# Kernel tuning notes

Hardware: AMD Instinct MI355X
Metric: run time of the kernel (lower is better)

Reference implementation:

```python
import jax, jax.numpy as jnp
import numpy as np

N, IN_FEATS, HIDDEN, N_CLASSES = 12000, 256, 256, 40
EPS = 1e-12  # F.normalize default eps


def setup_inputs() -> dict:
    key = jax.random.key(0)
    ks = jax.random.split(key, 6)
    # dense adjacency, scaled like a row-normalized graph operator
    adj = jax.random.uniform(ks[0], (N, N), jnp.float32) * (1.0 / 64.0)
    x = jax.random.normal(ks[1], (N, IN_FEATS), jnp.float32)
    # xavier-uniform-like weights, zero biases (matches init_params)
    def xavier(k, fan_in, fan_out):
        lim = np.sqrt(6.0 / (fan_in + fan_out)).astype(np.float32)
        return jax.random.uniform(k, (fan_in, fan_out), jnp.float32, -lim, lim)
    W0 = xavier(ks[2], IN_FEATS, HIDDEN)
    W1 = xavier(ks[3], HIDDEN, HIDDEN)
    W2 = xavier(ks[4], HIDDEN, N_CLASSES)
    b0 = jnp.zeros((HIDDEN,), jnp.float32)
    b1 = jnp.zeros((HIDDEN,), jnp.float32)
    b2 = jnp.zeros((N_CLASSES,), jnp.float32)
    return {"adj": adj, "x": x, "W0": W0, "b0": b0, "W1": W1, "b1": b1, "W2": W2, "b2": b2}


def _l2_normalize(h):
    # F.normalize(h): rows divided by max(||row||_2, eps)
    norm = jnp.sqrt(jnp.sum(h * h, axis=1, keepdims=True))
    return h / jnp.maximum(norm, EPS)


def reference(adj, x, W0, b0, W1, b1, W2, b2):
    # layer 0: aggregate -> linear -> bias -> relu -> l2-normalize (dropout=eval identity)
    h = _l2_normalize(jax.nn.relu((adj @ x) @ W0 + b0))
    # layer 1 (hidden)
    h = _l2_normalize(jax.nn.relu((adj @ h) @ W1 + b1))
    # output layer: no activation / normalize / dropout
    h = (adj @ h) @ W2 + b2
    return h
```

## Files before the change

### kernel.cpp

```cpp
#include <hip/hip_runtime.h>
#include <hip/hip_bf16.h>

#define M_ROWS 12000
#define K_PAD  12032
#define FEAT   256
#define NCLS   40
#define NSLICE 5
#define NTILES 188
#define NBM    47
#define PSLABE (M_ROWS * FEAT)
#define TILE_SHORTS 16384
#define HALF_SHORTS 8192

typedef __attribute__((ext_vector_type(4))) float f32x4;
typedef __attribute__((ext_vector_type(8))) short s16x8;
typedef __attribute__((ext_vector_type(4))) short s16x4;
typedef unsigned int u32;

__device__ __forceinline__ short f2bf(float f){
  __hip_bfloat16 h = __float2bfloat16(f);
  union { __hip_bfloat16 h; short s; } u; u.h = h; return u.s;
}
__device__ __forceinline__ float bf2f(short s){
  union { float f; u32 u; } v; v.u = ((u32)(unsigned short)s) << 16; return v.f;
}

__device__ __forceinline__ f32x4 mfma16(s16x8 a, s16x8 b, f32x4 c){
  return __builtin_amdgcn_mfma_f32_16x16x32_bf16(a, b, c, 0, 0, 0);
}

__device__ __forceinline__ void gl16(const void* g, void* l){
  __builtin_amdgcn_global_load_lds(
      (const __attribute__((address_space(1))) u32*)g,
      (__attribute__((address_space(3))) u32*)l, 16, 0, 0);
}

#define VM6   do { asm volatile("s_waitcnt vmcnt(6)" ::: "memory"); \
                   __builtin_amdgcn_sched_barrier(0); } while(0)
#define VM4   do { asm volatile("s_waitcnt vmcnt(4)" ::: "memory"); \
                   __builtin_amdgcn_sched_barrier(0); } while(0)
#define VM0   do { asm volatile("s_waitcnt vmcnt(0)" ::: "memory"); \
                   __builtin_amdgcn_sched_barrier(0); } while(0)
#define LGK0  do { asm volatile("s_waitcnt lgkmcnt(0)" ::: "memory"); \
                   __builtin_amdgcn_sched_barrier(0); } while(0)
#define BARR  do { __builtin_amdgcn_s_barrier(); \
                   __builtin_amdgcn_sched_barrier(0); } while(0)
#define SBAR  __builtin_amdgcn_sched_barrier(0)

__device__ __forceinline__ int swz(int r){ return (r & 3) ^ ((r >> 2) & 3); }

__global__ __launch_bounds__(256) void k_transpose_pack(const float* __restrict__ src,
                                                        short* __restrict__ Bpack){
  const int t = threadIdx.x;
  if (blockIdx.x == 375){
    short* d = Bpack + (size_t)187 * TILE_SHORTS + HALF_SHORTS + t * 32;
    s16x8 z = (s16x8)0;
    #pragma unroll
    for (int i = 0; i < 4; ++i) *(s16x8*)(d + 8*i) = z;
    return;
  }
  __shared__ float tile[32][257];
  const int r0 = blockIdx.x * 32;
  {
    const int r = t >> 3, cs = (t & 7) * 32;
    const float* s = src + (size_t)(r0 + r) * FEAT + cs;
    #pragma unroll
    for (int i = 0; i < 8; ++i){
      f32x4 v = *(const f32x4*)(s + 4*i);
      tile[r][cs + 4*i + 0] = v[0];
      tile[r][cs + 4*i + 1] = v[1];
      tile[r][cs + 4*i + 2] = v[2];
      tile[r][cs + 4*i + 3] = v[3];
    }
  }
  __syncthreads();
  const int c = t;
  const int kt = r0 >> 6, hh = (r0 >> 5) & 1, sc = swz(c);
  short* d = Bpack + (size_t)kt * TILE_SHORTS + hh * HALF_SHORTS + c * 32;
  #pragma unroll
  for (int i = 0; i < 4; ++i){
    s16x8 o;
    #pragma unroll
    for (int j = 0; j < 8; ++j) o[j] = f2bf(tile[8*i + j][c]);
    *(s16x8*)(d + ((i ^ sc) * 8)) = o;
  }
}

__global__ __launch_bounds__(512, 2) void k_gemm_l0(const float* __restrict__ adj,
                                                    const short* __restrict__ Bpack,
                                                    short* __restrict__ Apack,
                                                    short* __restrict__ Pbase){
  __shared__ __align__(16) short lds[2][4][8192];

  const int t = threadIdx.x;
  const int w = t >> 6, l = t & 63;
  const int wm = w >> 2, wn = w & 3;
  const int lr = l & 15, lg = l >> 4;

  int id = blockIdx.x;
  {
    const int xcd = id & 7, idx = id >> 3;
    id = (xcd < 3 ? xcd * 30 : 90 + (xcd - 3) * 29) + idx;
  }
  const int bm = id % NBM, s = id / NBM;
  const int row0 = bm * 256;
  const int u0  = (s < 3) ? s * 38 : 114 + (s - 3) * 37;
  const int nst = (s < 3) ? 38 : 37;

  const char* Bb = (const char*)Bpack;
  const size_t tp = (size_t)t * 16;
  short* Aw = Apack + (size_t)bm * NTILES * TILE_SHORTS;

  size_t abase[2];
  #pragma unroll
  for (int p = 0; p < 2; ++p){
    const int si = p * 512 + t;
    const int r  = si >> 2, sl = si & 3;
    int grow = row0 + r; if (grow > M_ROWS - 1) grow = M_ROWS - 1;
    abase[p] = (size_t)grow * M_ROWS + (size_t)((sl ^ swz(r)) * 8);
  }

  f32x4 av0[4], av1[4];

#define ISSUE_A0(kt) do{ \
    av0[0] = *(const f32x4*)(adj + abase[0] + (kt)*64);      \
    av0[1] = *(const f32x4*)(adj + abase[0] + (kt)*64 + 4);  \
    av0[2] = *(const f32x4*)(adj + abase[1] + (kt)*64);      \
    av0[3] = *(const f32x4*)(adj + abase[1] + (kt)*64 + 4); }while(0)
#define ISSUE_A1(kt) do{ \
    av1[0] = *(const f32x4*)(adj + abase[0] + (kt)*64 + 32);     \
    av1[1] = *(const f32x4*)(adj + abase[0] + (kt)*64 + 32 + 4); \
    av1[2] = *(const f32x4*)(adj + abase[1] + (kt)*64 + 32);     \
    av1[3] = *(const f32x4*)(adj + abase[1] + (kt)*64 + 32 + 4); }while(0)

#define CVT_WRITE_A(q, h, kt, AV) do{                                         \
    _Pragma("unroll")                                                         \
    for (int p = 0; p < 2; ++p){                                              \
      s16x8 o;                                                                \
      _Pragma("unroll")                                                       \
      for (int j = 0; j < 4; ++j){ o[j] = f2bf(AV[2*p][j]); o[4+j] = f2bf(AV[2*p+1][j]); } \
      const int si = p * 512 + t;                                             \
      *(s16x8*)&lds[q][h][si * 8] = o;                                        \
      *(s16x8*)(Aw + (size_t)(kt) * TILE_SHORTS + (h) * HALF_SHORTS + si * 8) = o; \
    } }while(0)

#define ST_BH(q, h, kt) do{                                                   \
    const char* s_ = Bb + (size_t)(kt) * 32768 + (h) * 16384 + tp;            \
    gl16(s_,        (char*)&lds[q][2+(h)][0] + w*1024);                       \
    gl16(s_ + 8192, (char*)&lds[q][2+(h)][0] + 8192 + w*1024); }while(0)

#define AF(q, h, mf) \
    (*(const s16x8*)&lds[q][h][ (wm*128 + (mf)*16 + lr) * 32 + \
      ((lg ^ swz(wm*128 + (mf)*16 + lr)) * 8) ])
#define BF(q, h, nf) \
    (*(const s16x8*)&lds[q][2+(h)][ (wn*64 + (nf)*16 + lr) * 32 + \
      ((lg ^ swz(wn*64 + (nf)*16 + lr)) * 8) ])

  f32x4 acc[8][4];
  #pragma unroll
  for (int m = 0; m < 8; ++m)
    #pragma unroll
    for (int n = 0; n < 4; ++n) acc[m][n] = (f32x4)(0.0f);

  ISSUE_A0(u0); ST_BH(0, 0, u0);
  ISSUE_A1(u0); ST_BH(0, 1, u0);
  VM6;  CVT_WRITE_A(0, 0, u0, av0);
  VM0;  CVT_WRITE_A(0, 1, u0, av1);
  LGK0;
  BARR;

  for (int t2 = 0; t2 < nst; ++t2){
    const int q = t2 & 1, qn = q ^ 1;
    const bool stg = (t2 + 1 < nst);
    const int ktn = u0 + t2 + 1;

    s16x8 bfr[4], af[4];

    #pragma unroll
    for (int n = 0; n < 4; ++n) bfr[n] = BF(q, 0, n);
    #pragma unroll
    for (int m = 0; m < 4; ++m) af[m] = AF(q, 0, m);
    if (stg){ ISSUE_A0(ktn); ST_BH(qn, 0, ktn); }
    BARR;
    __builtin_amdgcn_s_setprio(1);
    #pragma unroll
    for (int m = 0; m < 4; ++m)
      #pragma unroll
      for (int n = 0; n < 4; ++n)
        acc[m][n] = mfma16(af[m], bfr[n], acc[m][n]);
    __builtin_amdgcn_s_setprio(0);
    BARR;

    #pragma unroll
    for (int m = 0; m < 4; ++m) af[m] = AF(q, 0, m + 4);
    if (stg){ ISSUE_A1(ktn); ST_BH(qn, 1, ktn); }
    BARR;
    __builtin_amdgcn_s_setprio(1);
    #pragma unroll
    for (int m = 0; m < 4; ++m)
      #pragma unroll
      for (int n = 0; n < 4; ++n)
        acc[m + 4][n] = mfma16(af[m], bfr[n], acc[m + 4][n]);
    __builtin_amdgcn_s_setprio(0);
    BARR;

    #pragma unroll
    for (int n = 0; n < 4; ++n) bfr[n] = BF(q, 1, n);
    #pragma unroll
    for (int m = 0; m < 4; ++m) af[m] = AF(q, 1, m);
    if (stg){ VM6; CVT_WRITE_A(qn, 0, ktn, av0); }
    BARR;
    __builtin_amdgcn_s_setprio(1);
    #pragma unroll
    for (int m = 0; m < 4; ++m)
      #pragma unroll
      for (int n = 0; n < 4; ++n)
        acc[m][n] = mfma16(af[m], bfr[n], acc[m][n]);
    __builtin_amdgcn_s_setprio(0);
    BARR;

    #pragma unroll
    for (int m = 0; m < 4; ++m) af[m] = AF(q, 1, m + 4);
    if (stg){ VM0; CVT_WRITE_A(qn, 1, ktn, av1); }
    BARR;
    __builtin_amdgcn_s_setprio(1);
    #pragma unroll
    for (int m = 0; m < 4; ++m)
      #pragma unroll
      for (int n = 0; n < 4; ++n)
        acc[m + 4][n] = mfma16(af[m], bfr[n], acc[m + 4][n]);
    __builtin_amdgcn_s_setprio(0);
    if (stg) LGK0;
    BARR;
  }
#undef ISSUE_A0
#undef ISSUE_A1
#undef CVT_WRITE_A
#undef ST_BH
#undef AF
#undef BF

  short* P = Pbase + (size_t)s * PSLABE;
  #pragma unroll
  for (int m = 0; m < 8; ++m){
    const int row = row0 + wm*128 + m*16 + lg*4;
    #pragma unroll
    for (int n = 0; n < 4; ++n){
      const int col = wn*64 + n*16 + lr;
      short* pp = P + (size_t)row * FEAT + col;
      #pragma unroll
      for (int r = 0; r < 4; ++r)
        if (row + r < M_ROWS) pp[(size_t)r * FEAT] = f2bf(acc[m][n][r]);
    }
  }
}

__global__ __launch_bounds__(512, 2) void k_gemm_la2(const short* __restrict__ Apack,
                                                     const short* __restrict__ Bpack,
                                                     short* __restrict__ Pbase){
  __shared__ __align__(16) short Alds[3][16384];
  __shared__ __align__(16) short Blds[3][8192];

  const int t = threadIdx.x;
  const int w = t >> 6, l = t & 63;
  const int wm = w >> 2, wn = w & 3;
  const int lr = l & 15, lg = l >> 4;

  int id = blockIdx.x;
  {
    const int xcd = id & 7, idx = id >> 3;
    id = (xcd < 3 ? xcd * 30 : 90 + (xcd - 3) * 29) + idx;
  }
  const int bm = id % NBM, s = id / NBM;
  const int row0 = bm * 256;
  const int u0  = (s < 3) ? s * 38 : 114 + (s - 3) * 37;
  const int nst = (s < 3) ? 38 : 37;

  const char* Ab = (const char*)(Apack + (size_t)bm * NTILES * TILE_SHORTS);
  const char* Bb = (const char*)Bpack;
  const size_t tp = (size_t)t * 16;

#define ST_AH(buf, kt, h) do{                                                 \
    const char* s_ = Ab + (size_t)(kt) * 32768 + (h) * 16384 + tp;            \
    gl16(s_,        (char*)&Alds[buf][(h)*8192] + w*1024);                    \
    gl16(s_ + 8192, (char*)&Alds[buf][(h)*8192] + 8192 + w*1024); }while(0)
#define ST_BH(buf, kt, h) do{                                                 \
    const char* s_ = Bb + (size_t)(kt) * 32768 + (h) * 16384 + tp;            \
    gl16(s_,        (char*)&Blds[buf][0] + w*1024);                           \
    gl16(s_ + 8192, (char*)&Blds[buf][0] + 8192 + w*1024); }while(0)

#define AF(buf, h, mf) \
    (*(const s16x8*)&Alds[buf][ (h)*8192 + (wm*128 + (mf)*16 + lr) * 32 + \
      ((lg ^ swz(wm*128 + (mf)*16 + lr)) * 8) ])
#define BF(buf, nf) \
    (*(const s16x8*)&Blds[buf][ (wn*64 + (nf)*16 + lr) * 32 + \
      ((lg ^ swz(wn*64 + (nf)*16 + lr)) * 8) ])

  f32x4 acc[8][4];
  #pragma unroll
  for (int m = 0; m < 8; ++m)
    #pragma unroll
    for (int n = 0; n < 4; ++n) acc[m][n] = (f32x4)(0.0f);

  ST_AH(0, u0, 0); ST_AH(0, u0, 1);
  SBAR;
  ST_BH(0, u0, 0); ST_BH(1, u0, 1);
  SBAR;
  if (nst > 1){ ST_AH(1, u0 + 1, 0); ST_AH(1, u0 + 1, 1); VM4; }
  else        { VM0; }
  BARR;

  for (int t2 = 0; t2 < nst; ++t2){
    const int a0 = t2 % 3;
    const int b0 = (2*t2) % 3, b1 = (2*t2 + 1) % 3;
    const bool s1 = (t2 + 1 < nst), s2 = (t2 + 2 < nst);
    const int kt1 = u0 + t2 + 1, kt2 = u0 + t2 + 2;

    s16x8 bfr[4], af[8];

    #pragma unroll
    for (int n = 0; n < 4; ++n) bfr[n] = BF(b0, n);
    #pragma unroll
    for (int m = 0; m < 8; ++m) af[m] = AF(a0, 0, m);
    if (s1) ST_BH((2*t2 + 2) % 3, kt1, 0);
    BARR;
    __builtin_amdgcn_s_setprio(1);
    #pragma unroll
    for (int m = 0; m < 8; ++m)
      #pragma unroll
      for (int n = 0; n < 4; ++n)
        acc[m][n] = mfma16(af[m], bfr[n], acc[m][n]);
    __builtin_amdgcn_s_setprio(0);
    BARR;

    #pragma unroll
    for (int n = 0; n < 4; ++n) bfr[n] = BF(b1, n);
    #pragma unroll
    for (int m = 0; m < 8; ++m) af[m] = AF(a0, 1, m);
    if (s1) ST_BH((2*t2 + 3) % 3, kt1, 1);
    SBAR;
    if (s2){ ST_AH((t2 + 2) % 3, kt2, 0); ST_AH((t2 + 2) % 3, kt2, 1); }
    BARR;
    __builtin_amdgcn_s_setprio(1);
    #pragma unroll
    for (int m = 0; m < 8; ++m)
      #pragma unroll
      for (int n = 0; n < 4; ++n)
        acc[m][n] = mfma16(af[m], bfr[n], acc[m][n]);
    __builtin_amdgcn_s_setprio(0);
    if (s2)      { VM4; }
    else if (s1) { VM0; }
    BARR;
  }
#undef ST_AH
#undef ST_BH
#undef AF
#undef BF

  short* P = Pbase + (size_t)s * PSLABE;
  #pragma unroll
  for (int m = 0; m < 8; ++m){
    const int row = row0 + wm*128 + m*16 + lg*4;
    #pragma unroll
    for (int n = 0; n < 4; ++n){
      const int col = wn*64 + n*16 + lr;
      short* pp = P + (size_t)row * FEAT + col;
      #pragma unroll
      for (int r = 0; r < 4; ++r)
        if (row + r < M_ROWS) pp[(size_t)r * FEAT] = f2bf(acc[m][n][r]);
    }
  }
}

__global__ __launch_bounds__(256) void k_fused2(const short* __restrict__ Pb,
                                                const float* __restrict__ W,
                                                const float* __restrict__ b,
                                                short* __restrict__ Bpack){
  __shared__ float ylds[32][257];
  __shared__ float red[32][33];
  __shared__ float scale[32];
  const int t  = threadIdx.x;
  const int r0 = blockIdx.x * 32;
  {
    const int r = t >> 3, cs = (t & 7) * 32;
    const size_t off = (size_t)(r0 + r) * FEAT + cs;
    float aa[32];
    {
      const short* p0 = Pb + off;
      #pragma unroll
      for (int i4 = 0; i4 < 4; ++i4){
        s16x8 v = *(const s16x8*)(p0 + i4*8);
        #pragma unroll
        for (int e = 0; e < 8; ++e) aa[i4*8 + e] = bf2f(v[e]);
      }
    }
    #pragma unroll
    for (int s = 1; s < NSLICE; ++s){
      const short* ps = Pb + (size_t)s * PSLABE + off;
      #pragma unroll
      for (int i4 = 0; i4 < 4; ++i4){
        s16x8 v = *(const s16x8*)(ps + i4*8);
        #pragma unroll
        for (int e = 0; e < 8; ++e) aa[i4*8 + e] += bf2f(v[e]);
      }
    }
    #pragma unroll
    for (int k = 0; k < 32; ++k) ylds[r][cs + k] = aa[k];
  }
  __syncthreads();

  const int rg = t >> 5;
  const int cg = t & 31;
  float acc[4][8];
  {
    float bias[8];
    #pragma unroll
    for (int j = 0; j < 8; ++j) bias[j] = b[cg*8 + j];
    #pragma unroll
    for (int i = 0; i < 4; ++i)
      #pragma unroll
      for (int j = 0; j < 8; ++j) acc[i][j] = bias[j];
  }

  #pragma unroll 4
  for (int k = 0; k < FEAT; ++k){
    float yv[4];
    #pragma unroll
    for (int i = 0; i < 4; ++i) yv[i] = ylds[rg*4 + i][k];
    f32x4 w0 = *(const f32x4*)(W + (size_t)k * FEAT + cg*8);
    f32x4 w1 = *(const f32x4*)(W + (size_t)k * FEAT + cg*8 + 4);
    #pragma unroll
    for (int i = 0; i < 4; ++i){
      #pragma unroll
      for (int j = 0; j < 4; ++j){
        acc[i][j]     += yv[i] * w0[j];
        acc[i][4 + j] += yv[i] * w1[j];
      }
    }
  }

  #pragma unroll
  for (int i = 0; i < 4; ++i){
    float ss = 0.0f;
    #pragma unroll
    for (int j = 0; j < 8; ++j){
      float v = fmaxf(acc[i][j], 0.0f);
      acc[i][j] = v;
      ss += v * v;
    }
    red[rg*4 + i][cg] = ss;
  }
  __syncthreads();
  if (t < 32){
    float ssum = 0.0f;
    #pragma unroll
    for (int j = 0; j < 32; ++j) ssum += red[t][j];
    scale[t] = 1.0f / fmaxf(sqrtf(ssum), 1e-12f);
  }
  __syncthreads();

  float sc[4];
  #pragma unroll
  for (int i = 0; i < 4; ++i) sc[i] = scale[rg*4 + i];

  const int kb   = r0 + rg * 4;
  const int kt   = kb >> 6, hh = (kb >> 5) & 1, g = (kb >> 3) & 3, e0 = kb & 7;
  short* dbase = Bpack + (size_t)kt * TILE_SHORTS + hh * HALF_SHORTS;
  #pragma unroll
  for (int j = 0; j < 8; ++j){
    const int c = cg * 8 + j;
    s16x4 o;
    #pragma unroll
    for (int i = 0; i < 4; ++i) o[i] = f2bf(acc[i][j] * sc[i]);
    *(s16x4*)(dbase + c * 32 + ((g ^ swz(c)) * 8) + e0) = o;
  }
}

__global__ __launch_bounds__(256) void k_final2(const short* __restrict__ Pb,
                                                const float* __restrict__ W2,
                                                const float* __restrict__ b2,
                                                float* __restrict__ out){
  __shared__ float ylds[32][257];
  const int t  = threadIdx.x;
  const int r0 = blockIdx.x * 32;
  {
    const int r = t >> 3, cs = (t & 7) * 32;
    const size_t off = (size_t)(r0 + r) * FEAT + cs;
    float aa[32];
    {
      const short* p0 = Pb + off;
      #pragma unroll
      for (int i4 = 0; i4 < 4; ++i4){
        s16x8 v = *(const s16x8*)(p0 + i4*8);
        #pragma unroll
        for (int e = 0; e < 8; ++e) aa[i4*8 + e] = bf2f(v[e]);
      }
    }
    #pragma unroll
    for (int s = 1; s < NSLICE; ++s){
      const short* ps = Pb + (size_t)s * PSLABE + off;
      #pragma unroll
      for (int i4 = 0; i4 < 4; ++i4){
        s16x8 v = *(const s16x8*)(ps + i4*8);
        #pragma unroll
        for (int e = 0; e < 8; ++e) aa[i4*8 + e] += bf2f(v[e]);
      }
    }
    #pragma unroll
    for (int k = 0; k < 32; ++k) ylds[r][cs + k] = aa[k];
  }
  __syncthreads();

  #pragma unroll
  for (int e = t; e < 32 * NCLS; e += 256){
    const int r = e / NCLS, n = e % NCLS;
    float a = b2[n];
    #pragma unroll 8
    for (int k = 0; k < FEAT; ++k)
      a = fmaf(ylds[r][k], W2[(size_t)k * NCLS + n], a);
    out[(size_t)(r0 + r) * NCLS + n] = a;
  }
}

extern "C" void kernel_launch(void* const* d_in, const int* in_sizes, int n_in,
                              void* d_out, int out_size, void* d_ws, size_t ws_size,
                              hipStream_t stream){
  const float* adj = (const float*)d_in[0];
  const float* x   = (const float*)d_in[1];
  const float* W0  = (const float*)d_in[2];
  const float* b0  = (const float*)d_in[3];
  const float* W1  = (const float*)d_in[4];
  const float* b1  = (const float*)d_in[5];
  const float* W2  = (const float*)d_in[6];
  const float* b2  = (const float*)d_in[7];
  float* out = (float*)d_out;

  char* ws = (char*)d_ws;
  const size_t BPACK_BYTES = (size_t)NTILES * TILE_SHORTS * 2;
  const size_t APACK_BYTES = (size_t)NBM * NTILES * TILE_SHORTS * 2;

  short* Bpack = (short*)ws;
  short* Apack = (short*)(ws + BPACK_BYTES);
  short* P     = (short*)(ws + BPACK_BYTES + APACK_BYTES);

  const dim3 b256(256), b512(512);

  k_transpose_pack<<<376, b256, 0, stream>>>(x, Bpack);

  k_gemm_l0<<<NBM * NSLICE, b512, 0, stream>>>(adj, Bpack, Apack, P);
  k_fused2<<<375, b256, 0, stream>>>(P, W0, b0, Bpack);
  k_gemm_la2<<<NBM * NSLICE, b512, 0, stream>>>(Apack, Bpack, P);
  k_fused2<<<375, b256, 0, stream>>>(P, W1, b1, Bpack);
  k_gemm_la2<<<NBM * NSLICE, b512, 0, stream>>>(Apack, Bpack, P);
  k_final2<<<375, b256, 0, stream>>>(P, W2, b2, out);
}
```

Baseline: 526.8 us.

## Replace 256-row aggregation GEMM with 64-row tiles and relax layer-0 waits

Measured after the change: 659.7 us. +25.2%, slower.

```diff
diff --git a/kernel.cpp b/kernel.cpp
--- a/kernel.cpp
+++ b/kernel.cpp
@@ -39,13 +39,14 @@
                    __builtin_amdgcn_sched_barrier(0); } while(0)
 #define VM4   do { asm volatile("s_waitcnt vmcnt(4)" ::: "memory"); \
                    __builtin_amdgcn_sched_barrier(0); } while(0)
+#define VM1   do { asm volatile("s_waitcnt vmcnt(1)" ::: "memory"); \
+                   __builtin_amdgcn_sched_barrier(0); } while(0)
 #define VM0   do { asm volatile("s_waitcnt vmcnt(0)" ::: "memory"); \
                    __builtin_amdgcn_sched_barrier(0); } while(0)
 #define LGK0  do { asm volatile("s_waitcnt lgkmcnt(0)" ::: "memory"); \
                    __builtin_amdgcn_sched_barrier(0); } while(0)
 #define BARR  do { __builtin_amdgcn_s_barrier(); \
                    __builtin_amdgcn_sched_barrier(0); } while(0)
-#define SBAR  __builtin_amdgcn_sched_barrier(0)
 
 __device__ __forceinline__ int swz(int r){ return (r & 3) ^ ((r >> 2) & 3); }
 
@@ -165,7 +166,7 @@
   ISSUE_A0(u0); ST_BH(0, 0, u0);
   ISSUE_A1(u0); ST_BH(0, 1, u0);
   VM6;  CVT_WRITE_A(0, 0, u0, av0);
-  VM0;  CVT_WRITE_A(0, 1, u0, av1);
+  VM4;  CVT_WRITE_A(0, 1, u0, av1);
   LGK0;
   BARR;
 
@@ -204,11 +205,12 @@
     __builtin_amdgcn_s_setprio(0);
     BARR;
 
+    if (stg) { VM6; } else { VM4; }
     #pragma unroll
     for (int n = 0; n < 4; ++n) bfr[n] = BF(q, 1, n);
     #pragma unroll
     for (int m = 0; m < 4; ++m) af[m] = AF(q, 1, m);
-    if (stg){ VM6; CVT_WRITE_A(qn, 0, ktn, av0); }
+    if (stg){ CVT_WRITE_A(qn, 0, ktn, av0); }
     BARR;
     __builtin_amdgcn_s_setprio(1);
     #pragma unroll
@@ -221,7 +223,7 @@
 
     #pragma unroll
     for (int m = 0; m < 4; ++m) af[m] = AF(q, 1, m + 4);
-    if (stg){ VM0; CVT_WRITE_A(qn, 1, ktn, av1); }
+    if (stg){ VM4; CVT_WRITE_A(qn, 1, ktn, av1); }
     BARR;
     __builtin_amdgcn_s_setprio(1);
     #pragma unroll
@@ -255,115 +257,100 @@
   }
 }
 
-__global__ __launch_bounds__(512, 2) void k_gemm_la2(const short* __restrict__ Apack,
-                                                     const short* __restrict__ Bpack,
-                                                     short* __restrict__ Pbase){
-  __shared__ __align__(16) short Alds[3][16384];
-  __shared__ __align__(16) short Blds[3][8192];
+__global__ __launch_bounds__(256, 3) void k_gemm32(const short* __restrict__ Apack,
+                                                   const short* __restrict__ Bpack,
+                                                   short* __restrict__ Pbase){
+  __shared__ __align__(16) short Al[3][2048];
+  __shared__ __align__(16) short Bl[2][8192];
 
   const int t = threadIdx.x;
   const int w = t >> 6, l = t & 63;
-  const int wm = w >> 2, wn = w & 3;
   const int lr = l & 15, lg = l >> 4;
 
   int id = blockIdx.x;
   {
     const int xcd = id & 7, idx = id >> 3;
-    id = (xcd < 3 ? xcd * 30 : 90 + (xcd - 3) * 29) + idx;
-  }
-  const int bm = id % NBM, s = id / NBM;
-  const int row0 = bm * 256;
+    id = (xcd < 4 ? xcd * 118 : 472 + (xcd - 4) * 117) + idx;
+  }
+  const int mb = id % 188, s = id / 188;
+  const int bm = mb >> 2, qr = mb & 3;
+  const int row0 = mb * 64;
   const int u0  = (s < 3) ? s * 38 : 114 + (s - 3) * 37;
-  const int nst = (s < 3) ? 38 : 37;
-
-  const char* Ab = (const char*)(Apack + (size_t)bm * NTILES * TILE_SHORTS);
+  const int nstep = ((s < 3) ? 38 : 37) * 2;
+
+  const char* Aq = (const char*)(Apack + (size_t)bm * NTILES * TILE_SHORTS)
+                 + (size_t)qr * 4096;
   const char* Bb = (const char*)Bpack;
-  const size_t tp = (size_t)t * 16;
-
-#define ST_AH(buf, kt, h) do{                                                 \
-    const char* s_ = Ab + (size_t)(kt) * 32768 + (h) * 16384 + tp;            \
-    gl16(s_,        (char*)&Alds[buf][(h)*8192] + w*1024);                    \
-    gl16(s_ + 8192, (char*)&Alds[buf][(h)*8192] + 8192 + w*1024); }while(0)
-#define ST_BH(buf, kt, h) do{                                                 \
-    const char* s_ = Bb + (size_t)(kt) * 32768 + (h) * 16384 + tp;            \
-    gl16(s_,        (char*)&Blds[buf][0] + w*1024);                           \
-    gl16(s_ + 8192, (char*)&Blds[buf][0] + 8192 + w*1024); }while(0)
-
-#define AF(buf, h, mf) \
-    (*(const s16x8*)&Alds[buf][ (h)*8192 + (wm*128 + (mf)*16 + lr) * 32 + \
-      ((lg ^ swz(wm*128 + (mf)*16 + lr)) * 8) ])
-#define BF(buf, nf) \
-    (*(const s16x8*)&Blds[buf][ (wn*64 + (nf)*16 + lr) * 32 + \
-      ((lg ^ swz(wn*64 + (nf)*16 + lr)) * 8) ])
-
-  f32x4 acc[8][4];
-  #pragma unroll
-  for (int m = 0; m < 8; ++m)
+
+#define ST_A(buf, st_) do{                                                    \
+    const int kt_ = u0 + ((st_) >> 1), h_ = (st_) & 1;                        \
+    gl16(Aq + (size_t)kt_ * 32768 + h_ * 16384 + t * 16,                      \
+         (char*)&Al[buf][0] + w * 1024); }while(0)
+#define ST_B(buf, st_) do{                                                    \
+    const char* s_ = Bb + (size_t)(u0 + ((st_) >> 1)) * 32768                 \
+                   + ((st_) & 1) * 16384;                                     \
+    _Pragma("unroll")                                                         \
+    for (int j = 0; j < 4; ++j)                                               \
+      gl16(s_ + (j * 256 + t) * 16, (char*)&Bl[buf][0] + j * 4096 + w * 1024);\
+    }while(0)
+
+#define AF32(buf, mf) \
+    (*(const s16x8*)&Al[buf][ ((mf)*16 + lr) * 32 + \
+      ((lg ^ swz((mf)*16 + lr)) * 8) ])
+#define BF32(buf, nf) \
+    (*(const s16x8*)&Bl[buf][ (w*64 + (nf)*16 + lr) * 32 + \
+      ((lg ^ swz(w*64 + (nf)*16 + lr)) * 8) ])
+
+  f32x4 acc[4][4];
+  #pragma unroll
+  for (int m = 0; m < 4; ++m)
     #pragma unroll
     for (int n = 0; n < 4; ++n) acc[m][n] = (f32x4)(0.0f);
 
-  ST_AH(0, u0, 0); ST_AH(0, u0, 1);
-  SBAR;
-  ST_BH(0, u0, 0); ST_BH(1, u0, 1);
-  SBAR;
-  if (nst > 1){ ST_AH(1, u0 + 1, 0); ST_AH(1, u0 + 1, 1); VM4; }
-  else        { VM0; }
+  ST_A(0, 0);
+  ST_B(0, 0);
+  ST_A(1, 1);
+  VM1;
   BARR;
 
-  for (int t2 = 0; t2 < nst; ++t2){
-    const int a0 = t2 % 3;
-    const int b0 = (2*t2) % 3, b1 = (2*t2 + 1) % 3;
-    const bool s1 = (t2 + 1 < nst), s2 = (t2 + 2 < nst);
-    const int kt1 = u0 + t2 + 1, kt2 = u0 + t2 + 2;
-
-    s16x8 bfr[4], af[8];
-
-    #pragma unroll
-    for (int n = 0; n < 4; ++n) bfr[n] = BF(b0, n);
-    #pragma unroll
-    for (int m = 0; m < 8; ++m) af[m] = AF(a0, 0, m);
-    if (s1) ST_BH((2*t2 + 2) % 3, kt1, 0);
-    BARR;
+  for (int st = 0; st < nstep; ++st){
+    const int q  = st & 1;
+    const int ab = st % 3;
+    const bool s1 = (st + 1 < nstep), s2 = (st + 2 < nstep);
+
+    if (s1) ST_B(q ^ 1, st + 1);
+    if (s2) ST_A((st + 2) % 3, st + 2);
+
+    s16x8 bfr[4], af[4];
+    #pragma unroll
+    for (int n = 0; n < 4; ++n) bfr[n] = BF32(q, n);
+    #pragma unroll
+    for (int m = 0; m < 4; ++m) af[m] = AF32(ab, m);
+
     __builtin_amdgcn_s_setprio(1);
     #pragma unroll
-    for (int m = 0; m < 8; ++m)
+    for (int m = 0; m < 4; ++m)
       #pragma unroll
       for (int n = 0; n < 4; ++n)
         acc[m][n] = mfma16(af[m], bfr[n], acc[m][n]);
     __builtin_amdgcn_s_setprio(0);
-    BARR;
-
-    #pragma unroll
-    for (int n = 0; n < 4; ++n) bfr[n] = BF(b1, n);
-    #pragma unroll
-    for (int m = 0; m < 8; ++m) af[m] = AF(a0, 1, m);
-    if (s1) ST_BH((2*t2 + 3) % 3, kt1, 1);
-    SBAR;
-    if (s2){ ST_AH((t2 + 2) % 3, kt2, 0); ST_AH((t2 + 2) % 3, kt2, 1); }
-    BARR;
-    __builtin_amdgcn_s_setprio(1);
-    #pragma unroll
-    for (int m = 0; m < 8; ++m)
-      #pragma unroll
-      for (int n = 0; n < 4; ++n)
-        acc[m][n] = mfma16(af[m], bfr[n], acc[m][n]);
-    __builtin_amdgcn_s_setprio(0);
-    if (s2)      { VM4; }
+
+    if (s2)      { VM1; }
     else if (s1) { VM0; }
     BARR;
   }
-#undef ST_AH
-#undef ST_BH
-#undef AF
-#undef BF
+#undef ST_A
+#undef ST_B
+#undef AF32
+#undef BF32
 
   short* P = Pbase + (size_t)s * PSLABE;
   #pragma unroll
-  for (int m = 0; m < 8; ++m){
-    const int row = row0 + wm*128 + m*16 + lg*4;
+  for (int m = 0; m < 4; ++m){
+    const int row = row0 + m*16 + lg*4;
     #pragma unroll
     for (int n = 0; n < 4; ++n){
-      const int col = wn*64 + n*16 + lr;
+      const int col = w*64 + n*16 + lr;
       short* pp = P + (size_t)row * FEAT + col;
       #pragma unroll
       for (int r = 0; r < 4; ++r)
@@ -549,8 +536,8 @@
 
   k_gemm_l0<<<NBM * NSLICE, b512, 0, stream>>>(adj, Bpack, Apack, P);
   k_fused2<<<375, b256, 0, stream>>>(P, W0, b0, Bpack);
-  k_gemm_la2<<<NBM * NSLICE, b512, 0, stream>>>(Apack, Bpack, P);
+  k_gemm32<<<188 * NSLICE, b256, 0, stream>>>(Apack, Bpack, P);
   k_fused2<<<375, b256, 0, stream>>>(P, W1, b1, Bpack);
-  k_gemm_la2<<<NBM * NSLICE, b512, 0, stream>>>(Apack, Bpack, P);
+  k_gemm32<<<188 * NSLICE, b256, 0, stream>>>(Apack, Bpack, P);
   k_final2<<<375, b256, 0, stream>>>(P, W2, b2, out);
 }
```
